# Kernel tuning notes

Measured on AMD Instinct MI355X. Metric: run time of the kernel, lower is better.

The kernel has to match this reference:

```python
import jax, jax.numpy as jnp
import numpy as np
from jax import lax

# Model dims (mamba_ssm defaults: d_state=16, d_conv=4, expand=2, dt_rank=ceil(d_model/16))
V = 16384       # vocab_size
D = 1024        # embedding_dim / d_model
C_CLS = 128     # num_CLS_classes
D_INNER = 2 * D # expand * d_model = 2048
N = 16          # d_state
K = 4           # d_conv
DT_RANK = (D + 15) // 16  # 64
B, L = 4, 512


def setup_inputs() -> dict:
    key = jax.random.key(0)
    ks = jax.random.split(key, 12)
    s = 0.02
    tokens = jax.random.randint(ks[0], (B, L), 0, V, dtype=jnp.int64)
    embedding = jax.random.normal(ks[1], (V, D), jnp.float32) * s
    in_proj_w = jax.random.normal(ks[2], (2 * D_INNER, D), jnp.float32) * s
    conv_w = jax.random.normal(ks[3], (D_INNER, 1, K), jnp.float32) * 0.1
    conv_b = jnp.zeros((D_INNER,), jnp.float32)
    x_proj_w = jax.random.normal(ks[4], (DT_RANK + 2 * N, D_INNER), jnp.float32) * s
    dt_proj_w = jax.random.normal(ks[5], (D_INNER, DT_RANK), jnp.float32) * s
    dt_proj_b = jax.random.uniform(ks[6], (D_INNER,), jnp.float32, -4.0, -2.0)  # softplus -> small dt
    A_log = jnp.log(jnp.broadcast_to(jnp.arange(1, N + 1, dtype=jnp.float32), (D_INNER, N)))
    D_param = jnp.ones((D_INNER,), jnp.float32)
    out_proj_w = jax.random.normal(ks[7], (D, D_INNER), jnp.float32) * s
    recon_w = jax.random.normal(ks[8], (V, D), jnp.float32) * s
    cls_w = jax.random.normal(ks[9], (C_CLS, D), jnp.float32) * s
    return dict(tokens=tokens, embedding=embedding, in_proj_w=in_proj_w,
                conv_w=conv_w, conv_b=conv_b, x_proj_w=x_proj_w,
                dt_proj_w=dt_proj_w, dt_proj_b=dt_proj_b, A_log=A_log,
                D_param=D_param, out_proj_w=out_proj_w, recon_w=recon_w, cls_w=cls_w)


def _mamba(h, in_proj_w, conv_w, conv_b, x_proj_w, dt_proj_w, dt_proj_b, A_log, D_param, out_proj_w):
    # h: (B, L, D)
    xz = jnp.einsum('bld,ed->ble', h, in_proj_w)          # (B, L, 2*D_INNER)
    x, z = jnp.split(xz, 2, axis=-1)                      # each (B, L, D_INNER)
    # causal depthwise conv1d along L
    xt = jnp.swapaxes(x, 1, 2)                            # (B, D_INNER, L)
    xt = lax.conv_general_dilated(xt, conv_w, window_strides=(1,),
                                  padding=[(K - 1, 0)],
                                  feature_group_count=D_INNER,
                                  dimension_numbers=('NCH', 'OIH', 'NCH'))
    xt = xt + conv_b[None, :, None]
    x = jax.nn.silu(jnp.swapaxes(xt, 1, 2))               # (B, L, D_INNER)
    # input-dependent dt, B, C
    x_dbl = jnp.einsum('bld,ed->ble', x, x_proj_w)        # (B, L, DT_RANK+2N)
    dt, Bm, Cm = jnp.split(x_dbl, [DT_RANK, DT_RANK + N], axis=-1)
    delta = jax.nn.softplus(jnp.einsum('blr,dr->bld', dt, dt_proj_w) + dt_proj_b)  # (B,L,D_INNER)
    A = -jnp.exp(A_log)                                   # (D_INNER, N)
    dA = jnp.exp(delta[..., None] * A)                    # (B,L,D_INNER,N)
    dBx = delta[..., None] * Bm[:, :, None, :] * x[..., None]  # (B,L,D_INNER,N)
    # selective scan over time (sequential recurrence)
    dA_t = jnp.swapaxes(dA, 0, 1)                         # (L,B,D_INNER,N)
    dBx_t = jnp.swapaxes(dBx, 0, 1)
    C_t = jnp.swapaxes(Cm, 0, 1)                          # (L,B,N)
    def step(hc, inp):
        a, bx, c = inp
        hc = a * hc + bx                                  # (B,D_INNER,N)
        y = jnp.einsum('bdn,bn->bd', hc, c)
        return hc, y
    h0 = jnp.zeros((x.shape[0], D_INNER, N), x.dtype)
    _, ys = lax.scan(step, h0, (dA_t, dBx_t, C_t))
    y = jnp.swapaxes(ys, 0, 1) + x * D_param              # (B,L,D_INNER)
    y = y * jax.nn.silu(z)
    return jnp.einsum('ble,de->bld', y, out_proj_w)       # (B,L,D)


def reference(tokens, embedding, in_proj_w, conv_w, conv_b, x_proj_w,
              dt_proj_w, dt_proj_b, A_log, D_param, out_proj_w, recon_w, cls_w):
    h = embedding[tokens]                                 # (B,L,D)
    h = _mamba(h, in_proj_w, conv_w, conv_b, x_proj_w, dt_proj_w, dt_proj_b,
               A_log, D_param, out_proj_w)
    recon = jnp.einsum('bld,vd->blv', h, recon_w)         # (B,L,V)
    pooled = h.mean(axis=1)                               # mean CLS pooling assumption
    cls = jnp.einsum('bd,cd->bc', pooled, cls_w)          # (B,C_CLS)
    return (recon, cls)
```

## Files before the change

kernel.cpp:

```cpp
#include <hip/hip_runtime.h>
#include <hip/hip_bf16.h>
#include <stdint.h>

#define DIN    2048
#define MROWS  2048
#define LSEQ   512
#define NV     16384
#define DMODEL 1024
#define NC     8
#define CL     64

typedef __attribute__((ext_vector_type(8))) short bf16x8;
typedef __attribute__((ext_vector_type(4))) float f32x4;

__device__ __forceinline__ uint16_t f2bf(float f) {
  uint32_t u = __builtin_bit_cast(uint32_t, f);
  u += 0x7fffu + ((u >> 16) & 1u);
  return (uint16_t)(u >> 16);
}
__device__ __forceinline__ float bf2f(uint16_t u) {
  return __builtin_bit_cast(float, (uint32_t)u << 16);
}

__device__ __forceinline__ void gld_lds16(const uint16_t* g, uint16_t* l) {
  __builtin_amdgcn_global_load_lds(
      (const __attribute__((address_space(1))) void*)g,
      (__attribute__((address_space(3))) void*)l,
      16, 0, 0);
}

__global__ __launch_bounds__(512, 2) void gemm256_bf16_kernel(
    const uint16_t* __restrict__ A, const uint16_t* __restrict__ B,
    float* __restrict__ Cf, uint16_t* __restrict__ Cbf, int M, int N, int K)
{
  __shared__ uint16_t lds[4 * 16384];
  const int tid = threadIdx.x;
  const int w   = tid >> 6;
  const int l   = tid & 63;

  const int nwg = gridDim.x;
  const int cpx = nwg >> 3;
  const int swz = (blockIdx.x & 7) * cpx + (blockIdx.x >> 3);
  const int nmy = M >> 8;
  const int bm  = (swz % nmy) << 8;
  const int bn  = (swz / nmy) << 8;

  const int fr = l & 15;
  const int fg = l >> 4;
  const int wr = w >> 2;
  const int wc = w & 3;

  const int srow = l >> 2;
  const int kof  = (((l & 3) ^ ((l >> 3) & 3)) << 3);
  const int ar0  = (w * 2 + 0) * 16 + srow;
  const int ar1  = (w * 2 + 1) * 16 + srow;
  const uint16_t* Ag0 = A + (size_t)(bm + ar0) * K + kof;
  const uint16_t* Ag1 = A + (size_t)(bm + ar1) * K + kof;
  const uint16_t* Bg0 = B + (size_t)(bn + ar0) * K + kof;
  const uint16_t* Bg1 = B + (size_t)(bn + ar1) * K + kof;
  const int lA0 = (w * 2 + 0) * 512;
  const int lA1 = (w * 2 + 1) * 512;
  const int lB0 = 8192 + (w * 2 + 0) * 512;
  const int lB1 = 8192 + (w * 2 + 1) * 512;

  const int axr  = ((fg ^ ((fr >> 1) & 3)) << 3);
  const int aoff = (wr * 128 + fr) * 32 + axr;
  const int boff = 8192 + (wc * 64 + fr) * 32 + axr;

  f32x4 acc[8][4] = {};
  const int NT = K >> 5;

  auto stage_all = [&](int t) {
    const int sb = (t & 3) << 14;
    const int k0 = t << 5;
    gld_lds16(Ag0 + k0, lds + sb + lA0);
    gld_lds16(Ag1 + k0, lds + sb + lA1);
    gld_lds16(Bg0 + k0, lds + sb + lB0);
    gld_lds16(Bg1 + k0, lds + sb + lB1);
  };
  auto compute_full = [&](int sb) {
    bf16x8 af[8], bfr[4];
#pragma unroll
    for (int mi = 0; mi < 8; ++mi)
      af[mi] = *(const bf16x8*)(lds + sb + aoff + mi * 512);
#pragma unroll
    for (int ni = 0; ni < 4; ++ni)
      bfr[ni] = *(const bf16x8*)(lds + sb + boff + ni * 512);
    __builtin_amdgcn_s_setprio(1);
#pragma unroll
    for (int mi = 0; mi < 8; ++mi)
#pragma unroll
      for (int ni = 0; ni < 4; ++ni)
        acc[mi][ni] = __builtin_amdgcn_mfma_f32_16x16x32_bf16(af[mi], bfr[ni], acc[mi][ni], 0, 0, 0);
    __builtin_amdgcn_s_setprio(0);
  };

  stage_all(0); stage_all(1); stage_all(2);
  asm volatile("s_waitcnt vmcnt(8)" ::: "memory");
  __builtin_amdgcn_s_barrier();

  for (int t = 0; t < NT - 3; ++t) {
    const int sb = (t & 3) << 14;
    const int st = ((t + 3) & 3) << 14;
    const int k0 = (t + 3) << 5;
    bf16x8 af[8], bfr[4];
#pragma unroll
    for (int mi = 0; mi < 8; ++mi)
      af[mi] = *(const bf16x8*)(lds + sb + aoff + mi * 512);
    bfr[0] = *(const bf16x8*)(lds + sb + boff + 0 * 512);
    bfr[1] = *(const bf16x8*)(lds + sb + boff + 1 * 512);
    gld_lds16(Ag0 + k0, lds + st + lA0);
    gld_lds16(Ag1 + k0, lds + st + lA1);
    __builtin_amdgcn_s_barrier();
    asm volatile("s_waitcnt lgkmcnt(0)" ::: "memory");
    __builtin_amdgcn_sched_barrier(0);
    __builtin_amdgcn_s_setprio(1);
#pragma unroll
    for (int mi = 0; mi < 8; ++mi)
#pragma unroll
      for (int ni = 0; ni < 2; ++ni)
        acc[mi][ni] = __builtin_amdgcn_mfma_f32_16x16x32_bf16(af[mi], bfr[ni], acc[mi][ni], 0, 0, 0);
    __builtin_amdgcn_s_setprio(0);
    __builtin_amdgcn_s_barrier();
    bfr[2] = *(const bf16x8*)(lds + sb + boff + 2 * 512);
    bfr[3] = *(const bf16x8*)(lds + sb + boff + 3 * 512);
    gld_lds16(Bg0 + k0, lds + st + lB0);
    gld_lds16(Bg1 + k0, lds + st + lB1);
    __builtin_amdgcn_s_barrier();
    asm volatile("s_waitcnt lgkmcnt(0)" ::: "memory");
    __builtin_amdgcn_sched_barrier(0);
    __builtin_amdgcn_s_setprio(1);
#pragma unroll
    for (int mi = 0; mi < 8; ++mi)
#pragma unroll
      for (int ni = 2; ni < 4; ++ni)
        acc[mi][ni] = __builtin_amdgcn_mfma_f32_16x16x32_bf16(af[mi], bfr[ni], acc[mi][ni], 0, 0, 0);
    __builtin_amdgcn_s_setprio(0);
    asm volatile("s_waitcnt vmcnt(8)" ::: "memory");
    __builtin_amdgcn_s_barrier();
  }
  compute_full(((NT - 3) & 3) << 14);
  asm volatile("s_waitcnt vmcnt(4)" ::: "memory");
  __builtin_amdgcn_s_barrier();
  compute_full(((NT - 2) & 3) << 14);
  asm volatile("s_waitcnt vmcnt(0)" ::: "memory");
  __builtin_amdgcn_s_barrier();
  compute_full(((NT - 1) & 3) << 14);

#pragma unroll
  for (int mi = 0; mi < 8; ++mi) {
    const int r0 = bm + wr * 128 + mi * 16 + fg * 4;
#pragma unroll
    for (int ni = 0; ni < 4; ++ni) {
      const int c0 = bn + wc * 64 + ni * 16 + fr;
#pragma unroll
      for (int r = 0; r < 4; ++r) {
        const float v = acc[mi][ni][r];
        if (Cf)  Cf[(size_t)(r0 + r) * N + c0] = v;
        if (Cbf) Cbf[(size_t)(r0 + r) * N + c0] = f2bf(v);
      }
    }
  }
}

__global__ __launch_bounds__(256) void gemm_bf16_kernel(
    const uint16_t* __restrict__ A, const uint16_t* __restrict__ B,
    float* __restrict__ C, int M, int N, int K, int kchunk,
    const float* __restrict__ bias)
{
  __shared__ uint16_t As[128 * 32];
  __shared__ uint16_t Bs[128 * 32];
  const int tid  = threadIdx.x;
  const int wid  = tid >> 6;
  const int lane = tid & 63;
  const int bm = blockIdx.y * 128;
  const int bn = blockIdx.x * 128;
  const int k_beg = blockIdx.z * kchunk;
  float* Cout = C + (size_t)blockIdx.z * M * N;

  const int fr = lane & 15;
  const int fg = lane >> 4;
  const int wm = (wid >> 1) * 64;
  const int wn = (wid & 1) * 64;

  const int srow = wid * 32 + (lane >> 2);
  const int skof = (lane & 3) * 8;
  const uint16_t* Ag = A + (size_t)(bm + srow) * K + skof;
  const uint16_t* Bg = B + (size_t)(bn + srow) * K + skof;
  uint16_t* Al = As + wid * 1024;
  uint16_t* Bl = Bs + wid * 1024;

  f32x4 acc[4][4] = {};

  for (int k0 = 0; k0 < kchunk; k0 += 32) {
    const int kk = k_beg + k0;
    gld_lds16(Ag + kk, Al);
    gld_lds16(Ag + (size_t)16 * K + kk, Al + 512);
    gld_lds16(Bg + kk, Bl);
    gld_lds16(Bg + (size_t)16 * K + kk, Bl + 512);
    asm volatile("s_waitcnt vmcnt(0)" ::: "memory");
    __syncthreads();
    bf16x8 af[4], bfr[4];
#pragma unroll
    for (int i = 0; i < 4; ++i)
      af[i] = *(const bf16x8*)(As + (wm + i * 16 + fr) * 32 + fg * 8);
#pragma unroll
    for (int j = 0; j < 4; ++j)
      bfr[j] = *(const bf16x8*)(Bs + (wn + j * 16 + fr) * 32 + fg * 8);
#pragma unroll
    for (int i = 0; i < 4; ++i)
#pragma unroll
      for (int j = 0; j < 4; ++j)
        acc[i][j] = __builtin_amdgcn_mfma_f32_16x16x32_bf16(af[i], bfr[j], acc[i][j], 0, 0, 0);
    __syncthreads();
  }

#pragma unroll
  for (int i = 0; i < 4; ++i) {
    const int r0 = bm + wm + i * 16 + fg * 4;
#pragma unroll
    for (int j = 0; j < 4; ++j) {
      const int c0 = bn + wn + j * 16 + fr;
      const float bv = bias ? bias[c0] : 0.f;
#pragma unroll
      for (int r = 0; r < 4; ++r) {
        float v = acc[i][j][r];
        if (bias) {
          const float u = v + bv;
          v = (u > 20.f) ? u : log1pf(__expf(u));
        }
        Cout[(size_t)(r0 + r) * N + c0] = v;
      }
    }
  }
}

__global__ __launch_bounds__(256) void reduce4_dt_kernel(
    const float* __restrict__ in, float* __restrict__ xdbl, uint16_t* __restrict__ dtb) {
  const int i = blockIdx.x * 256 + threadIdx.x;
  const float s = in[i] + in[i + 262144] + in[i + 2 * 262144] + in[i + 3 * 262144];
  xdbl[i] = s;
  const int c = i & 127;
  if (c < 64) dtb[(i >> 7) * 64 + c] = f2bf(s);
}

__global__ __launch_bounds__(256) void reduce2_bf16_kernel(
    const float* __restrict__ in, uint16_t* __restrict__ outb, int n) {
  const int i = blockIdx.x * 256 + threadIdx.x;
  if (i >= n) return;
  outb[i] = f2bf(in[i] + in[i + (size_t)n]);
}

__global__ __launch_bounds__(256) void embed_kernel(
    const int* __restrict__ tok, const float* __restrict__ emb, uint16_t* __restrict__ out) {
  const int m = blockIdx.x;
  const int t = tok[m];
  const float4 v = ((const float4*)(emb + (size_t)t * DMODEL))[threadIdx.x];
  ((ushort4*)(out + (size_t)m * DMODEL))[threadIdx.x] =
      make_ushort4(f2bf(v.x), f2bf(v.y), f2bf(v.z), f2bf(v.w));
}

__global__ __launch_bounds__(256) void cvt_bf16_kernel(
    const float* __restrict__ in, uint16_t* __restrict__ out, int n4) {
  const int i = blockIdx.x * 256 + threadIdx.x;
  if (i >= n4) return;
  const float4 v = ((const float4*)in)[i];
  ((ushort4*)out)[i] = make_ushort4(f2bf(v.x), f2bf(v.y), f2bf(v.z), f2bf(v.w));
}

__global__ __launch_bounds__(256) void cvt_pad_kernel(
    const float* __restrict__ in, uint16_t* __restrict__ out, int rows_in, int cols4) {
  const int i = blockIdx.x * 256 + threadIdx.x;
  const int r = i / cols4, c = i % cols4;
  ushort4 o = make_ushort4(0, 0, 0, 0);
  if (r < rows_in) {
    const float4 v = ((const float4*)in)[(size_t)r * cols4 + c];
    o = make_ushort4(f2bf(v.x), f2bf(v.y), f2bf(v.z), f2bf(v.w));
  }
  ((ushort4*)out)[i] = o;
}

__global__ __launch_bounds__(256) void conv_silu_kernel(
    const float* __restrict__ xz, const float* __restrict__ cw, const float* __restrict__ cb,
    float* __restrict__ xc, uint16_t* __restrict__ xcb)
{
  const int idx = blockIdx.x * 256 + threadIdx.x;
  const int d = idx & (DIN - 1);
  const int m = idx >> 11;
  const int l = m & (LSEQ - 1);
  float acc = cb[d];
#pragma unroll
  for (int j = 0; j < 4; ++j) {
    const int lj = l - 3 + j;
    if (lj >= 0) acc += cw[d * 4 + j] * xz[(size_t)(m - 3 + j) * 4096 + d];
  }
  const float r = acc / (1.f + __expf(-acc));
  xc[idx] = r;
  xcb[idx] = f2bf(r);
}

__global__ __launch_bounds__(256) void scan_partial_kernel(
    const float* __restrict__ delta, const float* __restrict__ xc,
    const float* __restrict__ xdbl, const float* __restrict__ A_log,
    float* __restrict__ Pb, float* __restrict__ Qb)
{
  const int q = threadIdx.x & 3;
  const int d_idx = threadIdx.x >> 2;
  const int c = blockIdx.x;
  const int d = blockIdx.y * 64 + d_idx;
  const int b = blockIdx.z;
  float Arow[4];
#pragma unroll
  for (int n = 0; n < 4; ++n)
    Arow[n] = -expf(A_log[d * 16 + q * 4 + n]);
  float P[4] = {1.f, 1.f, 1.f, 1.f};
  float Q[4] = {0.f, 0.f, 0.f, 0.f};
  const int l0 = c * CL;
#pragma unroll 4
  for (int li = 0; li < CL; ++li) {
    const int m = b * LSEQ + l0 + li;
    const float de = delta[(size_t)m * DIN + d];
    const float xv = xc[(size_t)m * DIN + d];
    const float dx = de * xv;
    const float4 Bv = *(const float4*)(xdbl + (size_t)m * 128 + 64 + q * 4);
    const float bv[4] = {Bv.x, Bv.y, Bv.z, Bv.w};
#pragma unroll
    for (int n = 0; n < 4; ++n) {
      const float a = __expf(de * Arow[n]);
      P[n] *= a;
      Q[n] = a * Q[n] + dx * bv[n];
    }
  }
  const size_t o = ((size_t)(b * NC + c) * DIN + d) * 16 + q * 4;
  *(float4*)(Pb + o) = make_float4(P[0], P[1], P[2], P[3]);
  *(float4*)(Qb + o) = make_float4(Q[0], Q[1], Q[2], Q[3]);
}

__global__ __launch_bounds__(256) void scan_bounds_kernel(
    const float* __restrict__ Pb, const float* __restrict__ Qb, float* __restrict__ Hi)
{
  const int i = blockIdx.x * 256 + threadIdx.x;
  const int b = i >> 15;
  const int r = i & 32767;
  float h = 0.f;
#pragma unroll
  for (int c = 0; c < NC; ++c) {
    const size_t o = ((size_t)(b * NC + c) << 15) + r;
    Hi[o] = h;
    h = Pb[o] * h + Qb[o];
  }
}

__global__ __launch_bounds__(256) void scan_final_kernel(
    const float* __restrict__ delta, const float* __restrict__ xc,
    const float* __restrict__ xdbl, const float* __restrict__ xz,
    const float* __restrict__ A_log, const float* __restrict__ Dp,
    const float* __restrict__ Hi, uint16_t* __restrict__ yb)
{
  const int q = threadIdx.x & 3;
  const int d_idx = threadIdx.x >> 2;
  const int c = blockIdx.x;
  const int d = blockIdx.y * 64 + d_idx;
  const int b = blockIdx.z;
  float Arow[4];
#pragma unroll
  for (int n = 0; n < 4; ++n)
    Arow[n] = -expf(A_log[d * 16 + q * 4 + n]);
  const float dpd = Dp[d];
  const size_t o = ((size_t)(b * NC + c) * DIN + d) * 16 + q * 4;
  const float4 Hv = *(const float4*)(Hi + o);
  float h[4] = {Hv.x, Hv.y, Hv.z, Hv.w};
  const int l0 = c * CL;
#pragma unroll 2
  for (int li = 0; li < CL; ++li) {
    const int m = b * LSEQ + l0 + li;
    const float de = delta[(size_t)m * DIN + d];
    const float xv = xc[(size_t)m * DIN + d];
    const float dx = de * xv;
    const float4 Bv = *(const float4*)(xdbl + (size_t)m * 128 + 64 + q * 4);
    const float4 Cv = *(const float4*)(xdbl + (size_t)m * 128 + 80 + q * 4);
    const float bv[4] = {Bv.x, Bv.y, Bv.z, Bv.w};
    const float cv[4] = {Cv.x, Cv.y, Cv.z, Cv.w};
    float yp = 0.f;
#pragma unroll
    for (int n = 0; n < 4; ++n) {
      const float a = __expf(de * Arow[n]);
      h[n] = a * h[n] + dx * bv[n];
      yp += h[n] * cv[n];
    }
    yp += __shfl_xor(yp, 1);
    yp += __shfl_xor(yp, 2);
    if (q == 0) {
      const float z = xz[(size_t)m * 4096 + 2048 + d];
      const float sil = z / (1.f + __expf(-z));
      yb[(size_t)m * DIN + d] = f2bf((yp + xv * dpd) * sil);
    }
  }
}

__global__ __launch_bounds__(256) void pool1_kernel(
    const uint16_t* __restrict__ h2b, float* __restrict__ part) {
  const int b = blockIdx.x >> 4, s = blockIdx.x & 15;
  const int c = threadIdx.x * 4;
  const uint16_t* base = h2b + ((size_t)(b * LSEQ + s * 32)) * DMODEL + c;
  float a0 = 0, a1 = 0, a2 = 0, a3 = 0;
  for (int l = 0; l < 32; ++l) {
    const ushort4 v = *(const ushort4*)(base + (size_t)l * DMODEL);
    a0 += bf2f(v.x); a1 += bf2f(v.y); a2 += bf2f(v.z); a3 += bf2f(v.w);
  }
  *(float4*)(part + (size_t)blockIdx.x * DMODEL + c) = make_float4(a0, a1, a2, a3);
}

__global__ __launch_bounds__(256) void pool2_cls_kernel(
    const float* __restrict__ part, const float* __restrict__ w, float* __restrict__ out) {
  __shared__ float pl[DMODEL];
  const int b = blockIdx.x, t = threadIdx.x;
  float4 s = make_float4(0, 0, 0, 0);
  for (int k = 0; k < 16; ++k) {
    const float4 v = *(const float4*)(part + ((size_t)(b * 16 + k)) * DMODEL + t * 4);
    s.x += v.x; s.y += v.y; s.z += v.z; s.w += v.w;
  }
  const float inv = 1.f / (float)LSEQ;
  pl[t * 4 + 0] = s.x * inv; pl[t * 4 + 1] = s.y * inv;
  pl[t * 4 + 2] = s.z * inv; pl[t * 4 + 3] = s.w * inv;
  __syncthreads();
  if (t < 128) {
    const float* wr = w + (size_t)t * DMODEL;
    float acc = 0.f;
    for (int k = 0; k < DMODEL; ++k) acc += pl[k] * wr[k];
    out[b * 128 + t] = acc;
  }
}

extern "C" void kernel_launch(void* const* d_in, const int* in_sizes, int n_in,
                              void* d_out, int out_size, void* d_ws, size_t ws_size,
                              hipStream_t stream) {
  const int*   tokens    = (const int*)d_in[0];
  const float* embedding = (const float*)d_in[1];
  const float* in_proj_w = (const float*)d_in[2];
  const float* conv_w    = (const float*)d_in[3];
  const float* conv_b    = (const float*)d_in[4];
  const float* x_proj_w  = (const float*)d_in[5];
  const float* dt_proj_w = (const float*)d_in[6];
  const float* dt_proj_b = (const float*)d_in[7];
  const float* A_log     = (const float*)d_in[8];
  const float* D_param   = (const float*)d_in[9];
  const float* out_prj_w = (const float*)d_in[10];
  const float* recon_w   = (const float*)d_in[11];
  const float* cls_w     = (const float*)d_in[12];

  char* ws = (char*)d_ws;
  const size_t MB = 1024 * 1024;
  uint16_t* h_bf   = (uint16_t*)(ws + 0);
  uint16_t* w_in   = (uint16_t*)(ws + 4 * MB);
  float*    xz     = (float*)(ws + 12 * MB);
  float*    xc_f   = (float*)(ws + 44 * MB);
  uint16_t* xc_b   = (uint16_t*)(ws + 60 * MB);
  uint16_t* wx_bf  = (uint16_t*)(ws + 68 * MB);
  float*    xdbl   = (float*)(ws + 69 * MB);
  uint16_t* dt_bf  = (uint16_t*)(ws + 70 * MB);
  uint16_t* wdt_bf = (uint16_t*)(ws + 71 * MB);
  float*    delta  = (float*)(ws + 72 * MB);
  uint16_t* y_bf   = (uint16_t*)(ws + 88 * MB);
  uint16_t* h2_bf  = (uint16_t*)(ws + 96 * MB);
  float*    part   = (float*)(ws + 100 * MB);
  uint16_t* wout_bf = h_bf;
  uint16_t* wrec_bf = (uint16_t*)xz;
  float*    kscr    = delta;
  float*    Pbuf    = (float*)(ws + 60 * MB);
  float*    Qbuf    = (float*)(ws + 64 * MB);
  float*    Hinit   = (float*)(ws + 4 * MB);

  const int RECON = MROWS * NV;

  embed_kernel<<<dim3(MROWS), dim3(256), 0, stream>>>(tokens, embedding, h_bf);
  cvt_bf16_kernel<<<dim3(4096), dim3(256), 0, stream>>>(in_proj_w, w_in, 4096 * 1024 / 4);
  gemm256_bf16_kernel<<<dim3(128), dim3(512), 0, stream>>>(h_bf, w_in, xz, nullptr, MROWS, 4096, 1024);
  cvt_bf16_kernel<<<dim3(2048), dim3(256), 0, stream>>>(out_prj_w, wout_bf, 1024 * 2048 / 4);
  cvt_bf16_kernel<<<dim3(128), dim3(256), 0, stream>>>(dt_proj_w, wdt_bf, 2048 * 64 / 4);
  cvt_pad_kernel<<<dim3(256), dim3(256), 0, stream>>>(x_proj_w, wx_bf, 96, 512);
  conv_silu_kernel<<<dim3(16384), dim3(256), 0, stream>>>(xz, conv_w, conv_b, xc_f, xc_b);
  gemm_bf16_kernel<<<dim3(1, 16, 4), dim3(256), 0, stream>>>(xc_b, wx_bf, kscr, MROWS, 128, 2048, 512, nullptr);
  reduce4_dt_kernel<<<dim3(1024), dim3(256), 0, stream>>>(kscr, xdbl, dt_bf);
  gemm_bf16_kernel<<<dim3(16, 16, 1), dim3(256), 0, stream>>>(dt_bf, wdt_bf, delta, MROWS, DIN, 64, 64, dt_proj_b);
  scan_partial_kernel<<<dim3(NC, 32, 4), dim3(256), 0, stream>>>(delta, xc_f, xdbl, A_log, Pbuf, Qbuf);
  scan_bounds_kernel<<<dim3(512), dim3(256), 0, stream>>>(Pbuf, Qbuf, Hinit);
  scan_final_kernel<<<dim3(NC, 32, 4), dim3(256), 0, stream>>>(delta, xc_f, xdbl, xz, A_log, D_param, Hinit, y_bf);
  cvt_bf16_kernel<<<dim3(16384), dim3(256), 0, stream>>>(recon_w, wrec_bf, NV * 1024 / 4);
  gemm_bf16_kernel<<<dim3(8, 16, 2), dim3(256), 0, stream>>>(y_bf, wout_bf, kscr, MROWS, 1024, 2048, 1024, nullptr);
  reduce2_bf16_kernel<<<dim3(8192), dim3(256), 0, stream>>>(kscr, h2_bf, MROWS * 1024);
  gemm256_bf16_kernel<<<dim3(512), dim3(512), 0, stream>>>(h2_bf, wrec_bf, (float*)d_out, nullptr, MROWS, NV, 1024);
  pool1_kernel<<<dim3(64), dim3(256), 0, stream>>>(h2_bf, part);
  pool2_cls_kernel<<<dim3(4), dim3(256), 0, stream>>>(part, cls_w, (float*)d_out + RECON);
}
```

Measured before the change: 375.0 us.

## Simplify 256-tile GEMM loop, swizzle small-GEMM LDS, retune in_proj and x_proj splits

The 256x256 GEMM main loop drops its split A/B staging with interleaved barriers in favour of one stage call plus one full-tile compute per iteration, and loses the optional bf16 output. The 128-tile GEMM gains an XOR swizzle on the LDS column offset so fragment reads hit fewer bank conflicts. The in_proj GEMM moves from the 256-tile kernel with 128 blocks to the 128-tile kernel with 512 blocks to fill more CUs. The x_proj split-K goes from 4 to 8 chunks with a matching 8-way reduction. Together these trade finer-grained load/compute overlap in the large GEMM for simpler scheduling, and add more partial-sum traffic in exchange for parallelism in x_proj.

```diff
diff --git a/kernel.cpp b/kernel.cpp
--- a/kernel.cpp
+++ b/kernel.cpp
@@ -31,7 +31,7 @@
 
 __global__ __launch_bounds__(512, 2) void gemm256_bf16_kernel(
     const uint16_t* __restrict__ A, const uint16_t* __restrict__ B,
-    float* __restrict__ Cf, uint16_t* __restrict__ Cbf, int M, int N, int K)
+    float* __restrict__ C, int M, int N, int K)
 {
   __shared__ uint16_t lds[4 * 16384];
   const int tid = threadIdx.x;
@@ -70,7 +70,7 @@
   f32x4 acc[8][4] = {};
   const int NT = K >> 5;
 
-  auto stage_all = [&](int t) {
+  auto stage = [&](int t) {
     const int sb = (t & 3) << 14;
     const int k0 = t << 5;
     gld_lds16(Ag0 + k0, lds + sb + lA0);
@@ -78,7 +78,7 @@
     gld_lds16(Bg0 + k0, lds + sb + lB0);
     gld_lds16(Bg1 + k0, lds + sb + lB1);
   };
-  auto compute_full = [&](int sb) {
+  auto compute_tile = [&](int sb) {
     bf16x8 af[8], bfr[4];
 #pragma unroll
     for (int mi = 0; mi < 8; ++mi)
@@ -95,57 +95,23 @@
     __builtin_amdgcn_s_setprio(0);
   };
 
-  stage_all(0); stage_all(1); stage_all(2);
+  stage(0); stage(1); stage(2);
   asm volatile("s_waitcnt vmcnt(8)" ::: "memory");
   __builtin_amdgcn_s_barrier();
 
   for (int t = 0; t < NT - 3; ++t) {
-    const int sb = (t & 3) << 14;
-    const int st = ((t + 3) & 3) << 14;
-    const int k0 = (t + 3) << 5;
-    bf16x8 af[8], bfr[4];
-#pragma unroll
-    for (int mi = 0; mi < 8; ++mi)
-      af[mi] = *(const bf16x8*)(lds + sb + aoff + mi * 512);
-    bfr[0] = *(const bf16x8*)(lds + sb + boff + 0 * 512);
-    bfr[1] = *(const bf16x8*)(lds + sb + boff + 1 * 512);
-    gld_lds16(Ag0 + k0, lds + st + lA0);
-    gld_lds16(Ag1 + k0, lds + st + lA1);
-    __builtin_amdgcn_s_barrier();
-    asm volatile("s_waitcnt lgkmcnt(0)" ::: "memory");
-    __builtin_amdgcn_sched_barrier(0);
-    __builtin_amdgcn_s_setprio(1);
-#pragma unroll
-    for (int mi = 0; mi < 8; ++mi)
-#pragma unroll
-      for (int ni = 0; ni < 2; ++ni)
-        acc[mi][ni] = __builtin_amdgcn_mfma_f32_16x16x32_bf16(af[mi], bfr[ni], acc[mi][ni], 0, 0, 0);
-    __builtin_amdgcn_s_setprio(0);
-    __builtin_amdgcn_s_barrier();
-    bfr[2] = *(const bf16x8*)(lds + sb + boff + 2 * 512);
-    bfr[3] = *(const bf16x8*)(lds + sb + boff + 3 * 512);
-    gld_lds16(Bg0 + k0, lds + st + lB0);
-    gld_lds16(Bg1 + k0, lds + st + lB1);
-    __builtin_amdgcn_s_barrier();
-    asm volatile("s_waitcnt lgkmcnt(0)" ::: "memory");
-    __builtin_amdgcn_sched_barrier(0);
-    __builtin_amdgcn_s_setprio(1);
-#pragma unroll
-    for (int mi = 0; mi < 8; ++mi)
-#pragma unroll
-      for (int ni = 2; ni < 4; ++ni)
-        acc[mi][ni] = __builtin_amdgcn_mfma_f32_16x16x32_bf16(af[mi], bfr[ni], acc[mi][ni], 0, 0, 0);
-    __builtin_amdgcn_s_setprio(0);
+    stage(t + 3);
+    compute_tile((t & 3) << 14);
     asm volatile("s_waitcnt vmcnt(8)" ::: "memory");
     __builtin_amdgcn_s_barrier();
   }
-  compute_full(((NT - 3) & 3) << 14);
+  compute_tile(((NT - 3) & 3) << 14);
   asm volatile("s_waitcnt vmcnt(4)" ::: "memory");
   __builtin_amdgcn_s_barrier();
-  compute_full(((NT - 2) & 3) << 14);
+  compute_tile(((NT - 2) & 3) << 14);
   asm volatile("s_waitcnt vmcnt(0)" ::: "memory");
   __builtin_amdgcn_s_barrier();
-  compute_full(((NT - 1) & 3) << 14);
+  compute_tile(((NT - 1) & 3) << 14);
 
 #pragma unroll
   for (int mi = 0; mi < 8; ++mi) {
@@ -154,11 +120,8 @@
     for (int ni = 0; ni < 4; ++ni) {
       const int c0 = bn + wc * 64 + ni * 16 + fr;
 #pragma unroll
-      for (int r = 0; r < 4; ++r) {
-        const float v = acc[mi][ni][r];
-        if (Cf)  Cf[(size_t)(r0 + r) * N + c0] = v;
-        if (Cbf) Cbf[(size_t)(r0 + r) * N + c0] = f2bf(v);
-      }
+      for (int r = 0; r < 4; ++r)
+        C[(size_t)(r0 + r) * N + c0] = acc[mi][ni][r];
     }
   }
 }
@@ -184,11 +147,13 @@
   const int wn = (wid & 1) * 64;
 
   const int srow = wid * 32 + (lane >> 2);
-  const int skof = (lane & 3) * 8;
+  const int skof = (((lane & 3) ^ ((lane >> 2) & 3)) << 3);
   const uint16_t* Ag = A + (size_t)(bm + srow) * K + skof;
   const uint16_t* Bg = B + (size_t)(bn + srow) * K + skof;
   uint16_t* Al = As + wid * 1024;
   uint16_t* Bl = Bs + wid * 1024;
+
+  const int cxr = ((fg ^ (fr & 3)) << 3);
 
   f32x4 acc[4][4] = {};
 
@@ -203,10 +168,10 @@
     bf16x8 af[4], bfr[4];
 #pragma unroll
     for (int i = 0; i < 4; ++i)
-      af[i] = *(const bf16x8*)(As + (wm + i * 16 + fr) * 32 + fg * 8);
+      af[i] = *(const bf16x8*)(As + (wm + i * 16 + fr) * 32 + cxr);
 #pragma unroll
     for (int j = 0; j < 4; ++j)
-      bfr[j] = *(const bf16x8*)(Bs + (wn + j * 16 + fr) * 32 + fg * 8);
+      bfr[j] = *(const bf16x8*)(Bs + (wn + j * 16 + fr) * 32 + cxr);
 #pragma unroll
     for (int i = 0; i < 4; ++i)
 #pragma unroll
@@ -235,10 +200,12 @@
   }
 }
 
-__global__ __launch_bounds__(256) void reduce4_dt_kernel(
+__global__ __launch_bounds__(256) void reduce8_dt_kernel(
     const float* __restrict__ in, float* __restrict__ xdbl, uint16_t* __restrict__ dtb) {
   const int i = blockIdx.x * 256 + threadIdx.x;
-  const float s = in[i] + in[i + 262144] + in[i + 2 * 262144] + in[i + 3 * 262144];
+  float s = 0.f;
+#pragma unroll
+  for (int z = 0; z < 8; ++z) s += in[i + (size_t)z * 262144];
   xdbl[i] = s;
   const int c = i & 127;
   if (c < 64) dtb[(i >> 7) * 64 + c] = f2bf(s);
@@ -475,13 +442,13 @@
 
   embed_kernel<<<dim3(MROWS), dim3(256), 0, stream>>>(tokens, embedding, h_bf);
   cvt_bf16_kernel<<<dim3(4096), dim3(256), 0, stream>>>(in_proj_w, w_in, 4096 * 1024 / 4);
-  gemm256_bf16_kernel<<<dim3(128), dim3(512), 0, stream>>>(h_bf, w_in, xz, nullptr, MROWS, 4096, 1024);
+  gemm_bf16_kernel<<<dim3(32, 16, 1), dim3(256), 0, stream>>>(h_bf, w_in, xz, MROWS, 4096, 1024, 1024, nullptr);
   cvt_bf16_kernel<<<dim3(2048), dim3(256), 0, stream>>>(out_prj_w, wout_bf, 1024 * 2048 / 4);
   cvt_bf16_kernel<<<dim3(128), dim3(256), 0, stream>>>(dt_proj_w, wdt_bf, 2048 * 64 / 4);
   cvt_pad_kernel<<<dim3(256), dim3(256), 0, stream>>>(x_proj_w, wx_bf, 96, 512);
   conv_silu_kernel<<<dim3(16384), dim3(256), 0, stream>>>(xz, conv_w, conv_b, xc_f, xc_b);
-  gemm_bf16_kernel<<<dim3(1, 16, 4), dim3(256), 0, stream>>>(xc_b, wx_bf, kscr, MROWS, 128, 2048, 512, nullptr);
-  reduce4_dt_kernel<<<dim3(1024), dim3(256), 0, stream>>>(kscr, xdbl, dt_bf);
+  gemm_bf16_kernel<<<dim3(1, 16, 8), dim3(256), 0, stream>>>(xc_b, wx_bf, kscr, MROWS, 128, 2048, 256, nullptr);
+  reduce8_dt_kernel<<<dim3(1024), dim3(256), 0, stream>>>(kscr, xdbl, dt_bf);
   gemm_bf16_kernel<<<dim3(16, 16, 1), dim3(256), 0, stream>>>(dt_bf, wdt_bf, delta, MROWS, DIN, 64, 64, dt_proj_b);
   scan_partial_kernel<<<dim3(NC, 32, 4), dim3(256), 0, stream>>>(delta, xc_f, xdbl, A_log, Pbuf, Qbuf);
   scan_bounds_kernel<<<dim3(512), dim3(256), 0, stream>>>(Pbuf, Qbuf, Hinit);
@@ -489,7 +456,7 @@
   cvt_bf16_kernel<<<dim3(16384), dim3(256), 0, stream>>>(recon_w, wrec_bf, NV * 1024 / 4);
   gemm_bf16_kernel<<<dim3(8, 16, 2), dim3(256), 0, stream>>>(y_bf, wout_bf, kscr, MROWS, 1024, 2048, 1024, nullptr);
   reduce2_bf16_kernel<<<dim3(8192), dim3(256), 0, stream>>>(kscr, h2_bf, MROWS * 1024);
-  gemm256_bf16_kernel<<<dim3(512), dim3(512), 0, stream>>>(h2_bf, wrec_bf, (float*)d_out, nullptr, MROWS, NV, 1024);
+  gemm256_bf16_kernel<<<dim3(512), dim3(512), 0, stream>>>(h2_bf, wrec_bf, (float*)d_out, MROWS, NV, 1024);
   pool1_kernel<<<dim3(64), dim3(256), 0, stream>>>(h2_bf, part);
   pool2_cls_kernel<<<dim3(4), dim3(256), 0, stream>>>(part, cls_w, (float*)d_out + RECON);
 }
```

Result: faster. 363.3 us (-3.1%).
